# Kernel optimization log

Hardware: AMD Instinct MI355X
Metric: run time of the kernel (lower is better)

Reference implementation:

```python
import jax, jax.numpy as jnp
from jax import lax
import numpy as np

D, DI, S, K, R = 128, 256, 16, 4, 8  # d_model, d_inner, d_state, d_conv, dt_rank
B, W, N, E = 8, 64, 128, 256


def _ln(x, g, b, eps=1e-5):
    m = x.mean(-1, keepdims=True)
    v = ((x - m) ** 2).mean(-1, keepdims=True)
    return (x - m) * lax.rsqrt(v + eps) * g + b


def _mamba(x, w_in, conv_w, conv_b, w_xp, dt_w, dt_b, Alog, Dp, w_out):
    # x: (Bq, W, D) -> (Bq, W, D). Faithful mamba_ssm.Mamba math (selective scan).
    Bq, Wlen, _ = x.shape
    xz = x @ w_in                       # (Bq, W, 2*DI)
    xc, z = jnp.split(xz, 2, axis=-1)
    # causal depthwise conv over time
    xt = xc.transpose(0, 2, 1)          # (Bq, DI, W)
    xt = lax.conv_general_dilated(xt, conv_w[:, None, :], (1,), [(K - 1, 0)],
                                  feature_group_count=DI)
    xc = jax.nn.silu(xt + conv_b[None, :, None]).transpose(0, 2, 1)  # (Bq, W, DI)
    dbc = xc @ w_xp                     # (Bq, W, R+2S)
    dt = jax.nn.softplus(dbc[..., :R] @ dt_w + dt_b)   # (Bq, W, DI)
    Bm = dbc[..., R:R + S]              # (Bq, W, S)
    Cm = dbc[..., R + S:]               # (Bq, W, S)
    A = -jnp.exp(Alog)                  # (DI, S)

    def step(h, inp):
        dt_t, B_t, C_t, x_t = inp       # (Bq,DI),(Bq,S),(Bq,S),(Bq,DI)
        dA = jnp.exp(dt_t[..., None] * A)                 # (Bq,DI,S)
        h = dA * h + (dt_t * x_t)[..., None] * B_t[:, None, :]
        y = jnp.einsum('bds,bs->bd', h, C_t)
        return h, y

    h0 = jnp.zeros((Bq, DI, S), x.dtype)
    _, ys = lax.scan(step, h0, (dt.transpose(1, 0, 2), Bm.transpose(1, 0, 2),
                                Cm.transpose(1, 0, 2), xc.transpose(1, 0, 2)))
    y = ys.transpose(1, 0, 2) + xc * Dp          # D skip connection
    y = y * jax.nn.silu(z)
    return y @ w_out


def _forward(x_node, x_trace, x_log, mp_in, mp_conv_w, mp_conv_b, mp_xproj,
             mp_dt_w, mp_dt_b, mp_Alog, mp_D, mp_out, mix_w, mix_b,
             an_g, an_b, ff1_w, ff1_b, ff2_w, ff2_b, fln_g, fln_b):
    Bz, Wz, Nz, _ = x_node.shape
    Ez = x_trace.shape[2]
    # (B,W,N,D) -> (B*N, W, D) per-entity temporal sequences
    sn = x_node.transpose(0, 2, 1, 3).reshape(Bz * Nz, Wz, D)
    st = x_trace.transpose(0, 2, 1, 3).reshape(Bz * Ez, Wz, D)
    sl = x_log.transpose(0, 2, 1, 3).reshape(Bz * Nz, Wz, D)

    def mam(i, s):
        return _mamba(s, mp_in[i], mp_conv_w[i], mp_conv_b[i], mp_xproj[i],
                      mp_dt_w[i], mp_dt_b[i], mp_Alog[i], mp_D[i], mp_out[i])

    yn, yt, yl = mam(0, sn), mam(1, st), mam(2, sl)

    # cross-modal mixing of node & log with residual (dropout = identity in eval)
    cat = jnp.concatenate([yn, yl], axis=-1)          # (B*N, W, 2D)
    cat = cat + jax.nn.silu(cat @ mix_w + mix_b)
    yn, yl = jnp.split(cat, 2, axis=-1)

    # back to (B, W, N/E, D)
    yn = yn.reshape(Bz, Nz, Wz, D).transpose(0, 2, 1, 3)
    yt = yt.reshape(Bz, Ez, Wz, D).transpose(0, 2, 1, 3)
    yl = yl.reshape(Bz, Nz, Wz, D).transpose(0, 2, 1, 3)

    # AddALL: AddNorm(old, new) = LN(dropout(new) + old)
    n1 = _ln(yn + x_node, an_g[0], an_b[0])
    t1 = _ln(yt + x_trace, an_g[1], an_b[1])
    l1 = _ln(yl + x_log, an_g[2], an_b[2])

    # FFN: AddNorm(x, FeedForward(x)) per modality, LeakyReLU(0.01)
    def ffn(i, x):
        h = jax.nn.leaky_relu(x @ ff1_w[i] + ff1_b[i], 0.01)
        return _ln(h @ ff2_w[i] + ff2_b[i] + x, fln_g[i], fln_b[i])

    n2, t2, l2 = ffn(0, n1), ffn(1, t1), ffn(2, l1)
    # concat along entity axis (all feature dims = D) for a single output
    return jnp.concatenate([n2, t2, l2], axis=2)      # (B, W, 2N+E, D)


def setup_inputs() -> dict:
    key = jax.random.key(0)
    ks = jax.random.split(key, 16)
    f = lambda k, shp, s=1.0: jax.random.normal(k, shp, dtype=jnp.float32) * s
    return {
        'x_node': f(ks[0], (B, W, N, D)),
        'x_trace': f(ks[1], (B, W, E, D)),
        'x_log': f(ks[2], (B, W, N, D)),
        'mp_in': f(ks[3], (3, D, 2 * DI), 0.05),
        'mp_conv_w': f(ks[4], (3, DI, K), 0.2),
        'mp_conv_b': jnp.zeros((3, DI), jnp.float32),
        'mp_xproj': f(ks[5], (3, DI, R + 2 * S), 0.05),
        'mp_dt_w': f(ks[6], (3, R, DI), 0.1),
        'mp_dt_b': jnp.full((3, DI), float(np.log(np.expm1(0.01))), jnp.float32),
        'mp_Alog': jnp.log(jnp.broadcast_to(jnp.arange(1, S + 1, dtype=jnp.float32), (3, DI, S))),
        'mp_D': jnp.ones((3, DI), jnp.float32),
        'mp_out': f(ks[7], (3, DI, D), 0.05),
        'mix_w': f(ks[8], (2 * D, 2 * D), 0.05),
        'mix_b': jnp.zeros((2 * D,), jnp.float32),
        'an_g': jnp.ones((3, D), jnp.float32),
        'an_b': jnp.zeros((3, D), jnp.float32),
        'ff1_w': f(ks[9], (3, D, 4 * D), 0.05),
        'ff1_b': jnp.zeros((3, 4 * D), jnp.float32),
        'ff2_w': f(ks[10], (3, 4 * D, D), 0.05),
        'ff2_b': jnp.zeros((3, D), jnp.float32),
        'fln_g': jnp.ones((3, D), jnp.float32),
        'fln_b': jnp.zeros((3, D), jnp.float32),
    }


def reference(x_node, x_trace, x_log, mp_in, mp_conv_w, mp_conv_b, mp_xproj,
              mp_dt_w, mp_dt_b, mp_Alog, mp_D, mp_out, mix_w, mix_b,
              an_g, an_b, ff1_w, ff1_b, ff2_w, ff2_b, fln_g, fln_b):
    return _forward(x_node, x_trace, x_log, mp_in, mp_conv_w, mp_conv_b,
                    mp_xproj, mp_dt_w, mp_dt_b, mp_Alog, mp_D, mp_out,
                    mix_w, mix_b, an_g, an_b, ff1_w, ff1_b, ff2_w, ff2_b,
                    fln_g, fln_b)
```

## Files before the change

### kernel.cpp

```cpp
#include <hip/hip_runtime.h>

#define DEV __device__ __forceinline__

typedef __attribute__((ext_vector_type(8))) short bf16x8;
typedef __attribute__((ext_vector_type(4))) float f32x4;

DEV f32x4 MF(bf16x8 a, bf16x8 b, f32x4 c) {
  return __builtin_amdgcn_mfma_f32_16x16x32_bf16(a, b, c, 0, 0, 0);
}

DEV float bf2f(unsigned short u) {
  union { unsigned int i; float f; } v; v.i = ((unsigned int)u) << 16; return v.f;
}
DEV unsigned short f2bf(float f) {
  union { float f; unsigned int i; } v; v.f = f;
  unsigned int x = v.i;
  return (unsigned short)((x + 0x7fffu + ((x >> 16) & 1u)) >> 16);
}
#define LOG2E 1.442695041f
#define LN2   0.6931471806f
DEV float silu_fast(float v) {
  float e = __builtin_amdgcn_exp2f(v * -LOG2E);
  return v * __builtin_amdgcn_rcpf(1.f + e);
}
DEV float softplus_fast(float v) {
  float e = __builtin_amdgcn_exp2f(v * LOG2E);
  float l = __builtin_amdgcn_logf(1.f + e) * LN2;
  return v > 15.f ? v : l;
}

#define WS_WINT   0
#define WS_WXPT   196608
#define WS_WOUTT  233472
#define WS_FF1T   331776
#define WS_FF2T   528384
#define WS_MIXT   724992
#define WS_TOTAL  790528

__global__ __launch_bounds__(256) void prep_kernel(
    const float* __restrict__ w_in, const float* __restrict__ w_xp,
    const float* __restrict__ w_out, const float* __restrict__ ff1,
    const float* __restrict__ ff2, const float* __restrict__ mixw,
    unsigned short* __restrict__ ws)
{
  int idx = blockIdx.x * 256 + threadIdx.x;
  if (idx >= WS_TOTAL) return;
  float v;
  if (idx < WS_WXPT) {
    int j = idx, s = j / 65536, r = j % 65536, n = r >> 7, k = r & 127;
    v = w_in[s * 65536 + k * 512 + n];
  } else if (idx < WS_WOUTT) {
    int j = idx - WS_WXPT, s = j / 12288, r = j % 12288, n = r >> 8, k = r & 255;
    v = (n < 40) ? w_xp[s * 10240 + k * 40 + n] : 0.f;
  } else if (idx < WS_FF1T) {
    int j = idx - WS_WOUTT, s = j / 32768, r = j % 32768, n = r >> 8, k = r & 255;
    v = w_out[s * 32768 + k * 128 + n];
  } else if (idx < WS_FF2T) {
    int j = idx - WS_FF1T, s = j / 65536, r = j % 65536, n = r >> 7, k = r & 127;
    v = ff1[s * 65536 + k * 512 + n];
  } else if (idx < WS_MIXT) {
    int j = idx - WS_FF2T, s = j / 65536, r = j % 65536, n = r >> 9, k = r & 511;
    v = ff2[s * 65536 + k * 128 + n];
  } else {
    int j = idx - WS_MIXT, n = j >> 8, k = j & 255;
    v = mixw[k * 256 + n];
  }
  ws[idx] = f2bf(v);
}

__global__ __launch_bounds__(256, 2) void mamba_front(
    const float* __restrict__ xn, const float* __restrict__ xt,
    const float* __restrict__ xl,
    const unsigned short* __restrict__ w_inT_all,
    const float* __restrict__ conv_w_all, const float* __restrict__ conv_b_all,
    const unsigned short* __restrict__ w_xpT_all,
    const float* __restrict__ dt_w_all, const float* __restrict__ dt_b_all,
    const float* __restrict__ Alog_all, const float* __restrict__ Dp_all,
    const unsigned short* __restrict__ w_outT_all,
    const float* __restrict__ an_g, const float* __restrict__ an_b,
    float* __restrict__ out)
{
  __shared__ __attribute__((aligned(16))) unsigned short xcz[64 * 512];
  __shared__ __attribute__((aligned(16))) char aux[16384];
  unsigned short* xs = (unsigned short*)aux;
  float* dbc = (float*)aux;

  const int tid = threadIdx.x;
  const int lane = tid & 63;
  const int wv = tid >> 6;
  const int lr = lane & 15;
  const int kg = lane >> 4;

  int blk = blockIdx.x, s, q;
  if (blk < 1024)      { s = 0; q = blk; }
  else if (blk < 3072) { s = 1; q = blk - 1024; }
  else                 { s = 2; q = blk - 3072; }
  const int SEQ = (s == 1) ? 256 : 128;
  const int slot_base = (s == 0) ? 0 : (s == 1 ? 128 : 384);
  const float* x = (s == 0) ? xn : (s == 1 ? xt : xl);
  const unsigned short* w_inT  = w_inT_all  + (size_t)s * 65536;
  const unsigned short* w_xpT  = w_xpT_all  + (size_t)s * 12288;
  const unsigned short* w_outT = w_outT_all + (size_t)s * 32768;
  const float* conv_w = conv_w_all + s * 1024;
  const float* conv_b = conv_b_all + s * 256;
  const float* dt_w   = dt_w_all + s * 2048;
  const float* dt_b   = dt_b_all + s * 256;
  const float* Alog   = Alog_all + s * 4096;
  const float* Dp     = Dp_all + s * 256;

  const int b = q / SEQ, n = q - b * SEQ;
  const float* xb = x + ((size_t)b * 64 * SEQ + n) * 128;

  for (int idx = tid; idx < 2048; idx += 256) {
    int t = idx >> 5, qd = (idx & 31) << 2;
    float4 v = *(const float4*)(xb + (size_t)t * SEQ * 128 + qd);
    uint2 p;
    p.x = f2bf(v.x) | ((unsigned int)f2bf(v.y) << 16);
    p.y = f2bf(v.z) | ((unsigned int)f2bf(v.w) << 16);
    *(uint2*)(&xs[t * 128 + (qd ^ ((t & 7) << 3))]) = p;
  }
  __syncthreads();

  {
    bf16x8 bx[4][4];
#pragma unroll
    for (int jt = 0; jt < 4; ++jt)
#pragma unroll
      for (int ks = 0; ks < 4; ++ks) {
        int t = jt * 16 + lr;
        bx[jt][ks] = *(const bf16x8*)(&xs[t * 128 + ((ks * 32 + kg * 8) ^ ((t & 7) << 3))]);
      }
    const int nb = wv * 128;
#pragma unroll
    for (int at = 0; at < 8; ++at) {
      bf16x8 av[4];
      int arow = nb + at * 16 + lr;
#pragma unroll
      for (int ks = 0; ks < 4; ++ks)
        av[ks] = *(const bf16x8*)(w_inT + arow * 128 + ks * 32 + kg * 8);
#pragma unroll
      for (int jt = 0; jt < 4; ++jt) {
        f32x4 c = {0.f, 0.f, 0.f, 0.f};
#pragma unroll
        for (int ks = 0; ks < 4; ++ks) c = MF(av[ks], bx[jt][ks], c);
        int t = jt * 16 + lr;
        int n0 = nb + at * 16 + kg * 4;
        uint2 p;
        p.x = f2bf(c[0]) | ((unsigned int)f2bf(c[1]) << 16);
        p.y = f2bf(c[2]) | ((unsigned int)f2bf(c[3]) << 16);
        *(uint2*)(&xcz[t * 512 + (n0 ^ ((t & 7) << 3))]) = p;
      }
    }
  }
  __syncthreads();

  {
    const int d = tid;
    float cw0 = conv_w[d * 4 + 0], cw1 = conv_w[d * 4 + 1];
    float cw2 = conv_w[d * 4 + 2], cw3 = conv_w[d * 4 + 3];
    float cb = conv_b[d];
    float xm3 = 0.f, xm2 = 0.f, xm1 = 0.f;
    for (int c0 = 0; c0 < 64; c0 += 16) {
      float xv[16];
#pragma unroll
      for (int u = 0; u < 16; ++u) {
        int t = c0 + u;
        xv[u] = bf2f(xcz[t * 512 + (d ^ ((t & 7) << 3))]);
      }
#pragma unroll
      for (int u = 0; u < 16; ++u) {
        float sv = fmaf(cw0, xm3, fmaf(cw1, xm2, fmaf(cw2, xm1, fmaf(cw3, xv[u], cb))));
        xm3 = xm2; xm2 = xm1; xm1 = xv[u];
        xv[u] = silu_fast(sv);
      }
#pragma unroll
      for (int u = 0; u < 16; ++u) {
        int t = c0 + u;
        xcz[t * 512 + (d ^ ((t & 7) << 3))] = f2bf(xv[u]);
      }
    }
  }
  __syncthreads();

  {
    bf16x8 av[8];
    int ta = wv * 16 + lr;
#pragma unroll
    for (int ks = 0; ks < 8; ++ks)
      av[ks] = *(const bf16x8*)(&xcz[ta * 512 + ((ks * 32 + kg * 8) ^ ((ta & 7) << 3))]);
#pragma unroll
    for (int ct = 0; ct < 3; ++ct) {
      f32x4 c = {0.f, 0.f, 0.f, 0.f};
#pragma unroll
      for (int ks = 0; ks < 8; ++ks) {
        bf16x8 bv = *(const bf16x8*)(w_xpT + (ct * 16 + lr) * 256 + ks * 32 + kg * 8);
        c = MF(av[ks], bv, c);
      }
      int tt = wv * 16 + kg * 4;
#pragma unroll
      for (int r = 0; r < 4; ++r)
        dbc[(tt + r) * 48 + ct * 16 + lr] = c[r];
    }
  }
  __syncthreads();

  {
    const int d = tid;
    float dtw[8];
#pragma unroll
    for (int r = 0; r < 8; ++r) dtw[r] = dt_w[r * 256 + d];
    const float dtb = dt_b[d];
    float Af2[16];
#pragma unroll
    for (int s2 = 0; s2 < 16; ++s2)
      Af2[s2] = -__builtin_amdgcn_exp2f(Alog[d * 16 + s2] * LOG2E) * LOG2E;
    const float af0l2 = Af2[0];
    bool geo = true;
#pragma unroll
    for (int s2 = 1; s2 < 16; ++s2)
      geo = geo && (fabsf(Af2[s2] - (float)(s2 + 1) * af0l2) <= 1e-4f * fabsf(Af2[s2]));
    const float Dv = Dp[d];
    float h[16];
#pragma unroll
    for (int s2 = 0; s2 < 16; ++s2) h[s2] = 0.f;

    const int eoff = d;
    const int zoff = 256 + d;
    if (geo) {
#pragma unroll 2
      for (int t = 0; t < 64; ++t) {
        const float* dr = &dbc[t * 48];
        float dtv = dtb;
#pragma unroll
        for (int r = 0; r < 8; ++r) dtv = fmaf(dtw[r], dr[r], dtv);
        dtv = softplus_fast(dtv);
        int sw = (t & 7) << 3;
        int e = t * 512 + (eoff ^ sw);
        float xv = bf2f(xcz[e]);
        float zf = bf2f(xcz[t * 512 + (zoff ^ sw)]);
        float cf = dtv * xv;
        float r1 = __builtin_amdgcn_exp2f(dtv * af0l2);
        float p = 1.f, y = 0.f;
#pragma unroll
        for (int s2 = 0; s2 < 16; ++s2) {
          p *= r1;
          h[s2] = fmaf(p, h[s2], cf * dr[8 + s2]);
          y = fmaf(h[s2], dr[24 + s2], y);
        }
        xcz[e] = f2bf((y + xv * Dv) * silu_fast(zf));
      }
    } else {
#pragma unroll 2
      for (int t = 0; t < 64; ++t) {
        const float* dr = &dbc[t * 48];
        float dtv = dtb;
#pragma unroll
        for (int r = 0; r < 8; ++r) dtv = fmaf(dtw[r], dr[r], dtv);
        dtv = softplus_fast(dtv);
        int sw = (t & 7) << 3;
        int e = t * 512 + (eoff ^ sw);
        float xv = bf2f(xcz[e]);
        float zf = bf2f(xcz[t * 512 + (zoff ^ sw)]);
        float cf = dtv * xv;
        float y = 0.f;
#pragma unroll
        for (int s2 = 0; s2 < 16; ++s2) {
          float dA = __builtin_amdgcn_exp2f(dtv * Af2[s2]);
          h[s2] = fmaf(dA, h[s2], cf * dr[8 + s2]);
          y = fmaf(h[s2], dr[24 + s2], y);
        }
        xcz[e] = f2bf((y + xv * Dv) * silu_fast(zf));
      }
    }
  }
  __syncthreads();

  {
    bf16x8 av[8];
    int ta = wv * 16 + lr;
#pragma unroll
    for (int ks = 0; ks < 8; ++ks)
      av[ks] = *(const bf16x8*)(&xcz[ta * 512 + ((ks * 32 + kg * 8) ^ ((ta & 7) << 3))]);
    f32x4 acc[8];
#pragma unroll
    for (int ct = 0; ct < 8; ++ct) {
      f32x4 c = {0.f, 0.f, 0.f, 0.f};
#pragma unroll
      for (int ks = 0; ks < 8; ++ks) {
        bf16x8 bv = *(const bf16x8*)(w_outT + (ct * 16 + lr) * 256 + ks * 32 + kg * 8);
        c = MF(av[ks], bv, c);
      }
      acc[ct] = c;
    }
    size_t ob = (size_t)b * 64 * 512 * 128 + (size_t)(slot_base + n) * 128;
    const int trow = wv * 16 + kg * 4;
    if (s != 1) {
#pragma unroll
      for (int ct = 0; ct < 8; ++ct) {
        int cc = ct * 16 + lr;
#pragma unroll
        for (int r = 0; r < 4; ++r)
          out[ob + (size_t)(trow + r) * 65536 + cc] = acc[ct][r];
      }
    } else {
      float sum[4] = {0.f, 0.f, 0.f, 0.f}, sq[4] = {0.f, 0.f, 0.f, 0.f};
#pragma unroll
      for (int ct = 0; ct < 8; ++ct) {
        int col = ct * 16 + lr;
#pragma unroll
        for (int r = 0; r < 4; ++r) {
          int t = trow + r;
          float xr = xb[(size_t)t * SEQ * 128 + col];
          float v = acc[ct][r] + xr;
          acc[ct][r] = v;
          sum[r] += v; sq[r] += v * v;
        }
      }
      float mn[4], rstd[4];
#pragma unroll
      for (int r = 0; r < 4; ++r) {
        float s1 = sum[r], s2 = sq[r];
        s1 += __shfl_xor(s1, 1); s2 += __shfl_xor(s2, 1);
        s1 += __shfl_xor(s1, 2); s2 += __shfl_xor(s2, 2);
        s1 += __shfl_xor(s1, 4); s2 += __shfl_xor(s2, 4);
        s1 += __shfl_xor(s1, 8); s2 += __shfl_xor(s2, 8);
        float mean = s1 * (1.f / 128.f);
        float var = s2 * (1.f / 128.f) - mean * mean;
        mn[r] = mean;
        rstd[r] = rsqrtf(var + 1e-5f);
      }
      const float* G  = an_g + 128;
      const float* Bv = an_b + 128;
#pragma unroll
      for (int ct = 0; ct < 8; ++ct) {
        int col = ct * 16 + lr;
        float gc = G[col], bc = Bv[col];
#pragma unroll
        for (int r = 0; r < 4; ++r)
          out[ob + (size_t)(trow + r) * 65536 + col] = (acc[ct][r] - mn[r]) * rstd[r] * gc + bc;
      }
    }
  }
}

__global__ __launch_bounds__(256, 4) void mix_kernel(
    float* __restrict__ out, const unsigned short* __restrict__ mixT,
    const float* __restrict__ mix_b,
    const float* __restrict__ xn, const float* __restrict__ xl,
    const float* __restrict__ an_g, const float* __restrict__ an_b)
{
  __shared__ __attribute__((aligned(16))) unsigned short cs[64 * 256];

  const int tid = threadIdx.x;
  const int lane = tid & 63;
  const int wv = tid >> 6;
  const int lr = lane & 15;
  const int kg = lane >> 4;
  const int bn = blockIdx.x;
  const int b = bn >> 7, n = bn & 127;
  const size_t base_n = (((size_t)b * 64) * 512 + n) * 128;
  const size_t base_l = (((size_t)b * 64) * 512 + 384 + n) * 128;

  for (int idx = tid; idx < 4096; idx += 256) {
    int t = idx >> 6, r = idx & 63;
    int half = r >> 5, qd = (r & 31) << 2;
    const float* src = out + (half ? base_l : base_n) + (size_t)t * 65536 + qd;
    float4 v = *(const float4*)src;
    int col = half * 128 + qd;
    uint2 p;
    p.x = f2bf(v.x) | ((unsigned int)f2bf(v.y) << 16);
    p.y = f2bf(v.z) | ((unsigned int)f2bf(v.w) << 16);
    *(uint2*)(&cs[t * 256 + (col ^ ((t & 7) << 3))]) = p;
  }
  __syncthreads();

  bf16x8 av[8];
  int ta = wv * 16 + lr;
#pragma unroll
  for (int ks = 0; ks < 8; ++ks)
    av[ks] = *(const bf16x8*)(&cs[ta * 256 + ((ks * 32 + kg * 8) ^ ((ta & 7) << 3))]);

  const int trow = wv * 16 + kg * 4;
#pragma unroll
  for (int half = 0; half < 2; ++half) {
    const float* xres_base = half ? xl : xn;
    f32x4 acc[8];
#pragma unroll
    for (int ct = 0; ct < 8; ++ct) {
      f32x4 c = {0.f, 0.f, 0.f, 0.f};
      int colg = half * 128 + ct * 16 + lr;
#pragma unroll
      for (int ks = 0; ks < 8; ++ks) {
        bf16x8 bv = *(const bf16x8*)(mixT + colg * 256 + ks * 32 + kg * 8);
        c = MF(av[ks], bv, c);
      }
      acc[ct] = c;
    }
    float sum[4] = {0.f, 0.f, 0.f, 0.f}, sq[4] = {0.f, 0.f, 0.f, 0.f};
#pragma unroll
    for (int ct = 0; ct < 8; ++ct) {
      int col = ct * 16 + lr;
      int colg = half * 128 + col;
      float bcol = mix_b[colg];
#pragma unroll
      for (int r = 0; r < 4; ++r) {
        int t = trow + r;
        float orig = bf2f(cs[t * 256 + (colg ^ ((t & 7) << 3))]);
        float xr = xres_base[(((size_t)b * 64 + t) * 128 + n) * 128 + col];
        float v = orig + silu_fast(acc[ct][r] + bcol) + xr;
        acc[ct][r] = v;
        sum[r] += v; sq[r] += v * v;
      }
    }
    float mn[4], rstd[4];
#pragma unroll
    for (int r = 0; r < 4; ++r) {
      float s1 = sum[r], s2 = sq[r];
      s1 += __shfl_xor(s1, 1); s2 += __shfl_xor(s2, 1);
      s1 += __shfl_xor(s1, 2); s2 += __shfl_xor(s2, 2);
      s1 += __shfl_xor(s1, 4); s2 += __shfl_xor(s2, 4);
      s1 += __shfl_xor(s1, 8); s2 += __shfl_xor(s2, 8);
      float mean = s1 * (1.f / 128.f);
      float var = s2 * (1.f / 128.f) - mean * mean;
      mn[r] = mean;
      rstd[r] = rsqrtf(var + 1e-5f);
    }
    const float* G  = an_g + (half ? 256 : 0);
    const float* Bv = an_b + (half ? 256 : 0);
    size_t base = half ? base_l : base_n;
#pragma unroll
    for (int ct = 0; ct < 8; ++ct) {
      int col = ct * 16 + lr;
      float gc = G[col], bc = Bv[col];
#pragma unroll
      for (int r = 0; r < 4; ++r)
        out[base + (size_t)(trow + r) * 65536 + col] = (acc[ct][r] - mn[r]) * rstd[r] * gc + bc;
    }
  }
}

__global__ __launch_bounds__(256, 2) void ffn_kernel(
    float* __restrict__ out,
    const unsigned short* __restrict__ ff1T, const float* __restrict__ b1,
    const unsigned short* __restrict__ ff2T, const float* __restrict__ b2,
    const float* __restrict__ g, const float* __restrict__ bb)
{
  __shared__ __attribute__((aligned(16))) unsigned short hT[64 * 512];
  __shared__ __attribute__((aligned(16))) unsigned short xs[64 * 128];

  const int tid = threadIdx.x;
  const int lane = tid & 63;
  const int wv = tid >> 6;
  const int lr = lane & 15;
  const int kg = lane >> 4;
  const int tok0 = blockIdx.x * 64;
  const int slot0 = tok0 & 511;
  const int s = slot0 < 128 ? 0 : (slot0 < 384 ? 1 : 2);
  const unsigned short* F1 = ff1T + (size_t)s * 65536;
  const unsigned short* F2 = ff2T + (size_t)s * 65536;
  const float* B1 = b1 + s * 512;
  const float* B2 = b2 + s * 128;
  const float* G = g + s * 128;
  const float* Bb = bb + s * 128;

  for (int idx = tid; idx < 2048; idx += 256) {
    int t = idx >> 5, qd = (idx & 31) << 2;
    float4 v = *(const float4*)(out + (size_t)(tok0 + t) * 128 + qd);
    uint2 p;
    p.x = f2bf(v.x) | ((unsigned int)f2bf(v.y) << 16);
    p.y = f2bf(v.z) | ((unsigned int)f2bf(v.w) << 16);
    *(uint2*)(&xs[t * 128 + (qd ^ ((t & 7) << 3))]) = p;
  }
  __syncthreads();

  {
    bf16x8 bx[4][4];
#pragma unroll
    for (int jt = 0; jt < 4; ++jt)
#pragma unroll
      for (int ks = 0; ks < 4; ++ks) {
        int t = jt * 16 + lr;
        bx[jt][ks] = *(const bf16x8*)(&xs[t * 128 + ((ks * 32 + kg * 8) ^ ((t & 7) << 3))]);
      }
    const int nb = wv * 128;
#pragma unroll
    for (int at = 0; at < 8; ++at) {
      bf16x8 av[4];
      int arow = nb + at * 16 + lr;
#pragma unroll
      for (int ks = 0; ks < 4; ++ks)
        av[ks] = *(const bf16x8*)(F1 + arow * 128 + ks * 32 + kg * 8);
      float4 bias = *(const float4*)(B1 + nb + at * 16 + kg * 4);
#pragma unroll
      for (int jt = 0; jt < 4; ++jt) {
        f32x4 c = {0.f, 0.f, 0.f, 0.f};
#pragma unroll
        for (int ks = 0; ks < 4; ++ks) c = MF(av[ks], bx[jt][ks], c);
        float v0 = c[0] + bias.x; v0 = v0 > 0.f ? v0 : 0.01f * v0;
        float v1 = c[1] + bias.y; v1 = v1 > 0.f ? v1 : 0.01f * v1;
        float v2 = c[2] + bias.z; v2 = v2 > 0.f ? v2 : 0.01f * v2;
        float v3 = c[3] + bias.w; v3 = v3 > 0.f ? v3 : 0.01f * v3;
        int t = jt * 16 + lr;
        int n0 = nb + at * 16 + kg * 4;
        uint2 p;
        p.x = f2bf(v0) | ((unsigned int)f2bf(v1) << 16);
        p.y = f2bf(v2) | ((unsigned int)f2bf(v3) << 16);
        *(uint2*)(&hT[t * 512 + (n0 ^ ((t & 7) << 3))]) = p;
      }
    }
  }
  __syncthreads();

  {
    bf16x8 av[16];
    int ta = wv * 16 + lr;
#pragma unroll
    for (int ks = 0; ks < 16; ++ks)
      av[ks] = *(const bf16x8*)(&hT[ta * 512 + ((ks * 32 + kg * 8) ^ ((ta & 7) << 3))]);
    f32x4 acc[8];
#pragma unroll
    for (int ct = 0; ct < 8; ++ct) {
      f32x4 c = {0.f, 0.f, 0.f, 0.f};
#pragma unroll
      for (int ks = 0; ks < 16; ++ks) {
        bf16x8 bv = *(const bf16x8*)(F2 + (ct * 16 + lr) * 512 + ks * 32 + kg * 8);
        c = MF(av[ks], bv, c);
      }
      acc[ct] = c;
    }

    float v[8][4];
    float sum[4] = {0.f, 0.f, 0.f, 0.f}, sq[4] = {0.f, 0.f, 0.f, 0.f};
    const int trow = wv * 16 + kg * 4;
#pragma unroll
    for (int ct = 0; ct < 8; ++ct) {
      int col = ct * 16 + lr;
      float b2c = B2[col];
#pragma unroll
      for (int r = 0; r < 4; ++r) {
        int t = trow + r;
        float xr = bf2f(xs[t * 128 + (col ^ ((t & 7) << 3))]);
        float val = acc[ct][r] + b2c + xr;
        v[ct][r] = val;
        sum[r] += val; sq[r] += val * val;
      }
    }
    float mn[4], rstd[4];
#pragma unroll
    for (int r = 0; r < 4; ++r) {
      float s1 = sum[r], s2 = sq[r];
      s1 += __shfl_xor(s1, 1); s2 += __shfl_xor(s2, 1);
      s1 += __shfl_xor(s1, 2); s2 += __shfl_xor(s2, 2);
      s1 += __shfl_xor(s1, 4); s2 += __shfl_xor(s2, 4);
      s1 += __shfl_xor(s1, 8); s2 += __shfl_xor(s2, 8);
      float mean = s1 * (1.f / 128.f);
      float var = s2 * (1.f / 128.f) - mean * mean;
      mn[r] = mean;
      rstd[r] = rsqrtf(var + 1e-5f);
    }
#pragma unroll
    for (int ct = 0; ct < 8; ++ct) {
      int col = ct * 16 + lr;
      float gc = G[col], bc = Bb[col];
#pragma unroll
      for (int r = 0; r < 4; ++r)
        out[(size_t)(tok0 + trow + r) * 128 + col] = (v[ct][r] - mn[r]) * rstd[r] * gc + bc;
    }
  }
}

extern "C" void kernel_launch(void* const* d_in, const int* in_sizes, int n_in,
                              void* d_out, int out_size, void* d_ws, size_t ws_size,
                              hipStream_t stream) {
  (void)in_sizes; (void)n_in; (void)out_size; (void)ws_size;
  const float* x_node  = (const float*)d_in[0];
  const float* x_trace = (const float*)d_in[1];
  const float* x_log   = (const float*)d_in[2];
  const float* mp_in     = (const float*)d_in[3];
  const float* mp_conv_w = (const float*)d_in[4];
  const float* mp_conv_b = (const float*)d_in[5];
  const float* mp_xproj  = (const float*)d_in[6];
  const float* mp_dt_w   = (const float*)d_in[7];
  const float* mp_dt_b   = (const float*)d_in[8];
  const float* mp_Alog   = (const float*)d_in[9];
  const float* mp_D      = (const float*)d_in[10];
  const float* mp_out    = (const float*)d_in[11];
  const float* mix_w = (const float*)d_in[12];
  const float* mix_b = (const float*)d_in[13];
  const float* an_g  = (const float*)d_in[14];
  const float* an_b  = (const float*)d_in[15];
  const float* ff1_w = (const float*)d_in[16];
  const float* ff1_b = (const float*)d_in[17];
  const float* ff2_w = (const float*)d_in[18];
  const float* ff2_b = (const float*)d_in[19];
  const float* fln_g = (const float*)d_in[20];
  const float* fln_b = (const float*)d_in[21];
  float* out = (float*)d_out;

  unsigned short* ws = (unsigned short*)d_ws;

  prep_kernel<<<(WS_TOTAL + 255) / 256, 256, 0, stream>>>(
      mp_in, mp_xproj, mp_out, ff1_w, ff2_w, mix_w, ws);

  mamba_front<<<4096, 256, 0, stream>>>(
      x_node, x_trace, x_log,
      ws + WS_WINT, mp_conv_w, mp_conv_b, ws + WS_WXPT,
      mp_dt_w, mp_dt_b, mp_Alog, mp_D, ws + WS_WOUTT,
      an_g, an_b, out);

  mix_kernel<<<1024, 256, 0, stream>>>(out, ws + WS_MIXT, mix_b,
                                       x_node, x_log, an_g, an_b);

  ffn_kernel<<<4096, 256, 0, stream>>>(out, ws + WS_FF1T, ff1_b,
                                       ws + WS_FF2T, ff2_b, fln_g, fln_b);
}
```

Measured before the change: 819.7 us.

## Halve shared memory in mamba and FFN kernels to raise occupancy

The mamba kernel no longer keeps the z half of the in-projection in shared memory. Waves 2-3 hold z packed in registers, and the silu(z) gating moves to a separate pass after the scan, so the shared buffer shrinks from 64x512 to 64x256. The FFN kernel computes its hidden layer in two halves of 256 with an extra barrier per half, which also halves its hidden buffer. Both kernels raise their launch bound to 3 blocks per CU. The geometric scan path is vectorised with packed float2 FMAs. The trade-offs are 64 extra registers per thread for z, added syncs, and a looser tolerance on the geometric A check.

```diff
diff --git a/kernel.cpp b/kernel.cpp
--- a/kernel.cpp
+++ b/kernel.cpp
@@ -4,6 +4,7 @@
 
 typedef __attribute__((ext_vector_type(8))) short bf16x8;
 typedef __attribute__((ext_vector_type(4))) float f32x4;
+typedef __attribute__((ext_vector_type(2))) float f32x2;
 
 DEV f32x4 MF(bf16x8 a, bf16x8 b, f32x4 c) {
   return __builtin_amdgcn_mfma_f32_16x16x32_bf16(a, b, c, 0, 0, 0);
@@ -16,6 +17,9 @@
   union { float f; unsigned int i; } v; v.f = f;
   unsigned int x = v.i;
   return (unsigned short)((x + 0x7fffu + ((x >> 16) & 1u)) >> 16);
+}
+DEV unsigned int packbf(float a, float b) {
+  return (unsigned int)f2bf(a) | ((unsigned int)f2bf(b) << 16);
 }
 #define LOG2E 1.442695041f
 #define LN2   0.6931471806f
@@ -68,7 +72,7 @@
   ws[idx] = f2bf(v);
 }
 
-__global__ __launch_bounds__(256, 2) void mamba_front(
+__global__ __launch_bounds__(256, 3) void mamba_front(
     const float* __restrict__ xn, const float* __restrict__ xt,
     const float* __restrict__ xl,
     const unsigned short* __restrict__ w_inT_all,
@@ -80,7 +84,7 @@
     const float* __restrict__ an_g, const float* __restrict__ an_b,
     float* __restrict__ out)
 {
-  __shared__ __attribute__((aligned(16))) unsigned short xcz[64 * 512];
+  __shared__ __attribute__((aligned(16))) unsigned short xc[64 * 256];
   __shared__ __attribute__((aligned(16))) char aux[16384];
   unsigned short* xs = (unsigned short*)aux;
   float* dbc = (float*)aux;
@@ -111,44 +115,48 @@
   const int b = q / SEQ, n = q - b * SEQ;
   const float* xb = x + ((size_t)b * 64 * SEQ + n) * 128;
 
+  unsigned int zr[64];
+
   for (int idx = tid; idx < 2048; idx += 256) {
     int t = idx >> 5, qd = (idx & 31) << 2;
     float4 v = *(const float4*)(xb + (size_t)t * SEQ * 128 + qd);
     uint2 p;
-    p.x = f2bf(v.x) | ((unsigned int)f2bf(v.y) << 16);
-    p.y = f2bf(v.z) | ((unsigned int)f2bf(v.w) << 16);
+    p.x = packbf(v.x, v.y);
+    p.y = packbf(v.z, v.w);
     *(uint2*)(&xs[t * 128 + (qd ^ ((t & 7) << 3))]) = p;
   }
   __syncthreads();
 
   {
-    bf16x8 bx[4][4];
-#pragma unroll
-    for (int jt = 0; jt < 4; ++jt)
-#pragma unroll
-      for (int ks = 0; ks < 4; ++ks) {
-        int t = jt * 16 + lr;
-        bx[jt][ks] = *(const bf16x8*)(&xs[t * 128 + ((ks * 32 + kg * 8) ^ ((t & 7) << 3))]);
-      }
     const int nb = wv * 128;
 #pragma unroll
-    for (int at = 0; at < 8; ++at) {
-      bf16x8 av[4];
-      int arow = nb + at * 16 + lr;
+    for (int jt = 0; jt < 4; ++jt) {
+      int t = jt * 16 + lr;
+      int sw = (t & 7) << 3;
+      bf16x8 bxl[4];
 #pragma unroll
       for (int ks = 0; ks < 4; ++ks)
-        av[ks] = *(const bf16x8*)(w_inT + arow * 128 + ks * 32 + kg * 8);
-#pragma unroll
-      for (int jt = 0; jt < 4; ++jt) {
+        bxl[ks] = *(const bf16x8*)(&xs[t * 128 + ((ks * 32 + kg * 8) ^ sw)]);
+#pragma unroll
+      for (int at = 0; at < 8; ++at) {
+        bf16x8 av[4];
+        int arow = nb + at * 16 + lr;
+#pragma unroll
+        for (int ks = 0; ks < 4; ++ks)
+          av[ks] = *(const bf16x8*)(w_inT + arow * 128 + ks * 32 + kg * 8);
         f32x4 c = {0.f, 0.f, 0.f, 0.f};
 #pragma unroll
-        for (int ks = 0; ks < 4; ++ks) c = MF(av[ks], bx[jt][ks], c);
-        int t = jt * 16 + lr;
-        int n0 = nb + at * 16 + kg * 4;
-        uint2 p;
-        p.x = f2bf(c[0]) | ((unsigned int)f2bf(c[1]) << 16);
-        p.y = f2bf(c[2]) | ((unsigned int)f2bf(c[3]) << 16);
-        *(uint2*)(&xcz[t * 512 + (n0 ^ ((t & 7) << 3))]) = p;
+        for (int ks = 0; ks < 4; ++ks) c = MF(av[ks], bxl[ks], c);
+        if (wv < 2) {
+          int n0 = nb + at * 16 + kg * 4;
+          uint2 p;
+          p.x = packbf(c[0], c[1]);
+          p.y = packbf(c[2], c[3]);
+          *(uint2*)(&xc[t * 256 + (n0 ^ sw)]) = p;
+        } else {
+          zr[jt * 16 + at * 2 + 0] = packbf(c[0], c[1]);
+          zr[jt * 16 + at * 2 + 1] = packbf(c[2], c[3]);
+        }
       }
     }
   }
@@ -165,7 +173,7 @@
 #pragma unroll
       for (int u = 0; u < 16; ++u) {
         int t = c0 + u;
-        xv[u] = bf2f(xcz[t * 512 + (d ^ ((t & 7) << 3))]);
+        xv[u] = bf2f(xc[t * 256 + (d ^ ((t & 7) << 3))]);
       }
 #pragma unroll
       for (int u = 0; u < 16; ++u) {
@@ -176,7 +184,7 @@
 #pragma unroll
       for (int u = 0; u < 16; ++u) {
         int t = c0 + u;
-        xcz[t * 512 + (d ^ ((t & 7) << 3))] = f2bf(xv[u]);
+        xc[t * 256 + (d ^ ((t & 7) << 3))] = f2bf(xv[u]);
       }
     }
   }
@@ -187,7 +195,7 @@
     int ta = wv * 16 + lr;
 #pragma unroll
     for (int ks = 0; ks < 8; ++ks)
-      av[ks] = *(const bf16x8*)(&xcz[ta * 512 + ((ks * 32 + kg * 8) ^ ((ta & 7) << 3))]);
+      av[ks] = *(const bf16x8*)(&xc[ta * 256 + ((ks * 32 + kg * 8) ^ ((ta & 7) << 3))]);
 #pragma unroll
     for (int ct = 0; ct < 3; ++ct) {
       f32x4 c = {0.f, 0.f, 0.f, 0.f};
@@ -218,49 +226,59 @@
     bool geo = true;
 #pragma unroll
     for (int s2 = 1; s2 < 16; ++s2)
-      geo = geo && (fabsf(Af2[s2] - (float)(s2 + 1) * af0l2) <= 1e-4f * fabsf(Af2[s2]));
+      geo = geo && (fabsf(Af2[s2] - (float)(s2 + 1) * af0l2) <= 2e-4f * fabsf(Af2[s2]));
     const float Dv = Dp[d];
-    float h[16];
-#pragma unroll
-    for (int s2 = 0; s2 < 16; ++s2) h[s2] = 0.f;
-
-    const int eoff = d;
-    const int zoff = 256 + d;
+
     if (geo) {
+      f32x2 h2[8];
+#pragma unroll
+      for (int k = 0; k < 8; ++k) h2[k] = (f32x2){0.f, 0.f};
 #pragma unroll 2
+      for (int t = 0; t < 64; ++t) {
+        const f32x4* dr4 = (const f32x4*)&dbc[t * 48];
+        f32x4 d0 = dr4[0], d1 = dr4[1];
+        float dtv = dtb;
+        dtv = fmaf(dtw[0], d0[0], dtv); dtv = fmaf(dtw[1], d0[1], dtv);
+        dtv = fmaf(dtw[2], d0[2], dtv); dtv = fmaf(dtw[3], d0[3], dtv);
+        dtv = fmaf(dtw[4], d1[0], dtv); dtv = fmaf(dtw[5], d1[1], dtv);
+        dtv = fmaf(dtw[6], d1[2], dtv); dtv = fmaf(dtw[7], d1[3], dtv);
+        dtv = softplus_fast(dtv);
+        int e = t * 256 + (d ^ ((t & 7) << 3));
+        float xv = bf2f(xc[e]);
+        float cf = dtv * xv;
+        float r1 = __builtin_amdgcn_exp2f(dtv * af0l2);
+        float r2 = r1 * r1;
+        f32x2 r2v = {r2, r2};
+        f32x2 pp = {r1, r2};
+        f32x2 cf2 = {cf, cf};
+        f32x2 y2 = {0.f, 0.f};
+        f32x4 B0 = dr4[2], B1 = dr4[3], B2 = dr4[4], B3 = dr4[5];
+        f32x4 C0 = dr4[6], C1 = dr4[7], C2 = dr4[8], C3 = dr4[9];
+        f32x2 Bv[8] = {{B0[0],B0[1]},{B0[2],B0[3]},{B1[0],B1[1]},{B1[2],B1[3]},
+                       {B2[0],B2[1]},{B2[2],B2[3]},{B3[0],B3[1]},{B3[2],B3[3]}};
+        f32x2 Cv[8] = {{C0[0],C0[1]},{C0[2],C0[3]},{C1[0],C1[1]},{C1[2],C1[3]},
+                       {C2[0],C2[1]},{C2[2],C2[3]},{C3[0],C3[1]},{C3[2],C3[3]}};
+#pragma unroll
+        for (int k = 0; k < 8; ++k) {
+          h2[k] = __builtin_elementwise_fma(pp, h2[k], cf2 * Bv[k]);
+          y2 = __builtin_elementwise_fma(h2[k], Cv[k], y2);
+          pp = pp * r2v;
+        }
+        float y = y2[0] + y2[1];
+        xc[e] = f2bf(fmaf(xv, Dv, y));
+      }
+    } else {
+      float h[16];
+#pragma unroll
+      for (int s2 = 0; s2 < 16; ++s2) h[s2] = 0.f;
       for (int t = 0; t < 64; ++t) {
         const float* dr = &dbc[t * 48];
         float dtv = dtb;
 #pragma unroll
         for (int r = 0; r < 8; ++r) dtv = fmaf(dtw[r], dr[r], dtv);
         dtv = softplus_fast(dtv);
-        int sw = (t & 7) << 3;
-        int e = t * 512 + (eoff ^ sw);
-        float xv = bf2f(xcz[e]);
-        float zf = bf2f(xcz[t * 512 + (zoff ^ sw)]);
-        float cf = dtv * xv;
-        float r1 = __builtin_amdgcn_exp2f(dtv * af0l2);
-        float p = 1.f, y = 0.f;
-#pragma unroll
-        for (int s2 = 0; s2 < 16; ++s2) {
-          p *= r1;
-          h[s2] = fmaf(p, h[s2], cf * dr[8 + s2]);
-          y = fmaf(h[s2], dr[24 + s2], y);
-        }
-        xcz[e] = f2bf((y + xv * Dv) * silu_fast(zf));
-      }
-    } else {
-#pragma unroll 2
-      for (int t = 0; t < 64; ++t) {
-        const float* dr = &dbc[t * 48];
-        float dtv = dtb;
-#pragma unroll
-        for (int r = 0; r < 8; ++r) dtv = fmaf(dtw[r], dr[r], dtv);
-        dtv = softplus_fast(dtv);
-        int sw = (t & 7) << 3;
-        int e = t * 512 + (eoff ^ sw);
-        float xv = bf2f(xcz[e]);
-        float zf = bf2f(xcz[t * 512 + (zoff ^ sw)]);
+        int e = t * 256 + (d ^ ((t & 7) << 3));
+        float xv = bf2f(xc[e]);
         float cf = dtv * xv;
         float y = 0.f;
 #pragma unroll
@@ -269,7 +287,32 @@
           h[s2] = fmaf(dA, h[s2], cf * dr[8 + s2]);
           y = fmaf(h[s2], dr[24 + s2], y);
         }
-        xcz[e] = f2bf((y + xv * Dv) * silu_fast(zf));
+        xc[e] = f2bf(fmaf(xv, Dv, y));
+      }
+    }
+  }
+  __syncthreads();
+
+  if (wv >= 2) {
+    const int base_d = (wv - 2) * 128;
+#pragma unroll
+    for (int jt = 0; jt < 4; ++jt) {
+      int t = jt * 16 + lr;
+      int sw = (t & 7) << 3;
+#pragma unroll
+      for (int at = 0; at < 8; ++at) {
+#pragma unroll
+        for (int p = 0; p < 2; ++p) {
+          unsigned int zp = zr[jt * 16 + at * 2 + p];
+          int d0 = base_d + at * 16 + kg * 4 + p * 2;
+          int e0 = t * 256 + (d0 ^ sw);
+          unsigned int yv = *(unsigned int*)&xc[e0];
+          float y0 = bf2f((unsigned short)(yv & 0xffff));
+          float y1 = bf2f((unsigned short)(yv >> 16));
+          float z0 = bf2f((unsigned short)(zp & 0xffff));
+          float z1 = bf2f((unsigned short)(zp >> 16));
+          *(unsigned int*)&xc[e0] = packbf(y0 * silu_fast(z0), y1 * silu_fast(z1));
+        }
       }
     }
   }
@@ -280,7 +323,7 @@
     int ta = wv * 16 + lr;
 #pragma unroll
     for (int ks = 0; ks < 8; ++ks)
-      av[ks] = *(const bf16x8*)(&xcz[ta * 512 + ((ks * 32 + kg * 8) ^ ((ta & 7) << 3))]);
+      av[ks] = *(const bf16x8*)(&xc[ta * 256 + ((ks * 32 + kg * 8) ^ ((ta & 7) << 3))]);
     f32x4 acc[8];
 #pragma unroll
     for (int ct = 0; ct < 8; ++ct) {
@@ -368,8 +411,8 @@
     float4 v = *(const float4*)src;
     int col = half * 128 + qd;
     uint2 p;
-    p.x = f2bf(v.x) | ((unsigned int)f2bf(v.y) << 16);
-    p.y = f2bf(v.z) | ((unsigned int)f2bf(v.w) << 16);
+    p.x = packbf(v.x, v.y);
+    p.y = packbf(v.z, v.w);
     *(uint2*)(&cs[t * 256 + (col ^ ((t & 7) << 3))]) = p;
   }
   __syncthreads();
@@ -439,13 +482,13 @@
   }
 }
 
-__global__ __launch_bounds__(256, 2) void ffn_kernel(
+__global__ __launch_bounds__(256, 3) void ffn_kernel(
     float* __restrict__ out,
     const unsigned short* __restrict__ ff1T, const float* __restrict__ b1,
     const unsigned short* __restrict__ ff2T, const float* __restrict__ b2,
     const float* __restrict__ g, const float* __restrict__ bb)
 {
-  __shared__ __attribute__((aligned(16))) unsigned short hT[64 * 512];
+  __shared__ __attribute__((aligned(16))) unsigned short hT[64 * 256];
   __shared__ __attribute__((aligned(16))) unsigned short xs[64 * 128];
 
   const int tid = threadIdx.x;
@@ -467,24 +510,31 @@
     int t = idx >> 5, qd = (idx & 31) << 2;
     float4 v = *(const float4*)(out + (size_t)(tok0 + t) * 128 + qd);
     uint2 p;
-    p.x = f2bf(v.x) | ((unsigned int)f2bf(v.y) << 16);
-    p.y = f2bf(v.z) | ((unsigned int)f2bf(v.w) << 16);
+    p.x = packbf(v.x, v.y);
+    p.y = packbf(v.z, v.w);
     *(uint2*)(&xs[t * 128 + (qd ^ ((t & 7) << 3))]) = p;
   }
   __syncthreads();
 
-  {
-    bf16x8 bx[4][4];
-#pragma unroll
-    for (int jt = 0; jt < 4; ++jt)
-#pragma unroll
-      for (int ks = 0; ks < 4; ++ks) {
-        int t = jt * 16 + lr;
-        bx[jt][ks] = *(const bf16x8*)(&xs[t * 128 + ((ks * 32 + kg * 8) ^ ((t & 7) << 3))]);
-      }
-    const int nb = wv * 128;
-#pragma unroll
-    for (int at = 0; at < 8; ++at) {
+  bf16x8 bx[4][4];
+#pragma unroll
+  for (int jt = 0; jt < 4; ++jt)
+#pragma unroll
+    for (int ks = 0; ks < 4; ++ks) {
+      int t = jt * 16 + lr;
+      bx[jt][ks] = *(const bf16x8*)(&xs[t * 128 + ((ks * 32 + kg * 8) ^ ((t & 7) << 3))]);
+    }
+
+  f32x4 acc[8];
+#pragma unroll
+  for (int ct = 0; ct < 8; ++ct) acc[ct] = (f32x4){0.f, 0.f, 0.f, 0.f};
+
+  const int ta = wv * 16 + lr;
+#pragma unroll
+  for (int half = 0; half < 2; ++half) {
+    const int nb = half * 256 + wv * 64;
+#pragma unroll
+    for (int at = 0; at < 4; ++at) {
       bf16x8 av[4];
       int arow = nb + at * 16 + lr;
 #pragma unroll
@@ -501,34 +551,33 @@
         float v2 = c[2] + bias.z; v2 = v2 > 0.f ? v2 : 0.01f * v2;
         float v3 = c[3] + bias.w; v3 = v3 > 0.f ? v3 : 0.01f * v3;
         int t = jt * 16 + lr;
-        int n0 = nb + at * 16 + kg * 4;
+        int nl = wv * 64 + at * 16 + kg * 4;
         uint2 p;
-        p.x = f2bf(v0) | ((unsigned int)f2bf(v1) << 16);
-        p.y = f2bf(v2) | ((unsigned int)f2bf(v3) << 16);
-        *(uint2*)(&hT[t * 512 + (n0 ^ ((t & 7) << 3))]) = p;
-      }
-    }
-  }
-  __syncthreads();
+        p.x = packbf(v0, v1);
+        p.y = packbf(v2, v3);
+        *(uint2*)(&hT[t * 256 + (nl ^ ((t & 7) << 3))]) = p;
+      }
+    }
+    __syncthreads();
+
+    bf16x8 av2[8];
+#pragma unroll
+    for (int ks = 0; ks < 8; ++ks)
+      av2[ks] = *(const bf16x8*)(&hT[ta * 256 + ((ks * 32 + kg * 8) ^ ((ta & 7) << 3))]);
+#pragma unroll
+    for (int ct = 0; ct < 8; ++ct) {
+      f32x4 c = acc[ct];
+#pragma unroll
+      for (int ks = 0; ks < 8; ++ks) {
+        bf16x8 bv = *(const bf16x8*)(F2 + (ct * 16 + lr) * 512 + half * 256 + ks * 32 + kg * 8);
+        c = MF(av2[ks], bv, c);
+      }
+      acc[ct] = c;
+    }
+    __syncthreads();
+  }
 
   {
-    bf16x8 av[16];
-    int ta = wv * 16 + lr;
-#pragma unroll
-    for (int ks = 0; ks < 16; ++ks)
-      av[ks] = *(const bf16x8*)(&hT[ta * 512 + ((ks * 32 + kg * 8) ^ ((ta & 7) << 3))]);
-    f32x4 acc[8];
-#pragma unroll
-    for (int ct = 0; ct < 8; ++ct) {
-      f32x4 c = {0.f, 0.f, 0.f, 0.f};
-#pragma unroll
-      for (int ks = 0; ks < 16; ++ks) {
-        bf16x8 bv = *(const bf16x8*)(F2 + (ct * 16 + lr) * 512 + ks * 32 + kg * 8);
-        c = MF(av[ks], bv, c);
-      }
-      acc[ct] = c;
-    }
-
     float v[8][4];
     float sum[4] = {0.f, 0.f, 0.f, 0.f}, sq[4] = {0.f, 0.f, 0.f, 0.f};
     const int trow = wv * 16 + kg * 4;
```

New measurement: 883.5 us. 7.8% more time.
